# Kernel optimization log

Hardware: AMD Instinct MI355X
Metric: run time of the kernel (lower is better)

The kernel has to match this reference:

```python
import jax, jax.numpy as jnp
import numpy as np

NUM_CLASSES = 4096
FEAT_DIM = 2048
BATCH = 8192


def setup_inputs() -> dict:
    key = jax.random.key(0)
    kx, kl, kc = jax.random.split(key, 3)
    x = jax.random.normal(kx, (BATCH, FEAT_DIM), dtype=jnp.float32)
    labels = jax.random.randint(kl, (BATCH,), 0, NUM_CLASSES, dtype=jnp.int64)
    centers = jax.random.normal(kc, (NUM_CLASSES, FEAT_DIM), dtype=jnp.float32)
    return {"x": x, "labels": labels, "centers": centers}


def reference(x, labels, centers):
    # distmat[b, c] = ||x_b||^2 + ||center_c||^2 - 2 x_b . center_c
    xf = x.astype(jnp.float32)
    cf = centers.astype(jnp.float32)
    x_sq = jnp.sum(xf * xf, axis=1, keepdims=True)          # (B, 1)
    c_sq = jnp.sum(cf * cf, axis=1)[None, :]                 # (1, C)
    distmat = x_sq + c_sq - 2.0 * (xf @ cf.T)                # (B, C)
    # keep only the entry matching each sample's label class
    mask = (labels[:, None] == jnp.arange(NUM_CLASSES)[None, :]).astype(jnp.float32)
    dist = distmat * mask
    # NOTE: torch clamps the masked matrix, so zeroed entries become 1e-12 and
    # still contribute to the sum — replicated faithfully here.
    loss = jnp.clip(dist, 1e-12, 1e12).sum() / x.shape[0]
    return loss
```

## Files before the change

kernel.cpp:

```cpp
#include <hip/hip_runtime.h>


#define BATCH 8192
#define FEAT  2048
#define NCLS  4096
#define BLK   256
#define WAVES_PER_BLK (BLK / 64)
#define NPART (BATCH / WAVES_PER_BLK)

__global__ void __launch_bounds__(BLK)
cl_dist(const float* __restrict__ x,
        const int* __restrict__ labels,
        const float* __restrict__ centers,
        float* __restrict__ part) {
    const int tid  = threadIdx.x;
    const int wid  = tid >> 6;
    const int lane = tid & 63;
    const int b    = blockIdx.x * WAVES_PER_BLK + wid;

    const int lbl = labels[b];

    const float4* __restrict__ xr =
        reinterpret_cast<const float4*>(x + (size_t)b * FEAT);
    const float4* __restrict__ cr =
        reinterpret_cast<const float4*>(centers + (size_t)lbl * FEAT);

    float acc0 = 0.0f, acc1 = 0.0f;
#pragma unroll
    for (int j = 0; j < FEAT / 4 / 64; ++j) {
        const int idx = lane + j * 64;
        const float4 xv = xr[idx];
        const float4 cv = cr[idx];
        const float d0 = xv.x - cv.x;
        const float d1 = xv.y - cv.y;
        const float d2 = xv.z - cv.z;
        const float d3 = xv.w - cv.w;
        acc0 += d0 * d0 + d1 * d1;
        acc1 += d2 * d2 + d3 * d3;
    }
    float acc = acc0 + acc1;

#pragma unroll
    for (int off = 32; off > 0; off >>= 1)
        acc += __shfl_down(acc, off, 64);

    __shared__ float s[WAVES_PER_BLK];
    if (lane == 0) {
        s[wid] = fminf(fmaxf(acc, 1e-12f), 1e12f);
    }
    __syncthreads();

    if (tid == 0)
        part[blockIdx.x] = s[0] + s[1] + s[2] + s[3];
}

__global__ void __launch_bounds__(BLK)
cl_final(const float* __restrict__ part, float* __restrict__ out) {
    const int tid = threadIdx.x;
    float acc = 0.0f;
#pragma unroll
    for (int j = 0; j < NPART / BLK; ++j)
        acc += part[tid + j * BLK];

#pragma unroll
    for (int off = 32; off > 0; off >>= 1)
        acc += __shfl_down(acc, off, 64);

    __shared__ float s[BLK / 64];
    const int wid  = tid >> 6;
    const int lane = tid & 63;
    if (lane == 0) s[wid] = acc;
    __syncthreads();

    if (tid == 0) {
        const float total = s[0] + s[1] + s[2] + s[3];
        out[0] = total / (float)BATCH + (float)(NCLS - 1) * 1e-12f;
    }
}

extern "C" void kernel_launch(void* const* d_in, const int* in_sizes, int n_in,
                              void* d_out, int out_size, void* d_ws, size_t ws_size,
                              hipStream_t stream) {
    const float* x       = (const float*)d_in[0];
    const int*   labels  = (const int*)d_in[1];
    const float* centers = (const float*)d_in[2];
    float* out  = (float*)d_out;
    float* part = (float*)d_ws;

    cl_dist<<<NPART, BLK, 0, stream>>>(x, labels, centers, part);
    cl_final<<<1, BLK, 0, stream>>>(part, out);
}
```

Before: 25.95 us.

## Fuse distance and final reduction into one kernel with spin-wait consumer block

Merges the two kernels into one launch. Block 0 spin-waits with atomic loads and s_sleep on a per-sample partial array, zeroed by a hipMemsetAsync, and sums entries as the producer blocks write their clamped per-sample distances. This removes the second kernel launch and its gap, but adds a memset, polling traffic, and a reliance on nonzero sentinels and forward-progress scheduling of block 0.

```diff
diff --git a/kernel.cpp b/kernel.cpp
--- a/kernel.cpp
+++ b/kernel.cpp
@@ -6,18 +6,48 @@
 #define NCLS  4096
 #define BLK   256
 #define WAVES_PER_BLK (BLK / 64)
-#define NPART (BATCH / WAVES_PER_BLK)
+#define NWBLK (BATCH / WAVES_PER_BLK)
+#define NBLK  (NWBLK + 1)
+#define PER_THREAD (BATCH / BLK)
 
 __global__ void __launch_bounds__(BLK)
-cl_dist(const float* __restrict__ x,
-        const int* __restrict__ labels,
-        const float* __restrict__ centers,
-        float* __restrict__ part) {
+cl_all(const float* __restrict__ x,
+       const int* __restrict__ labels,
+       const float* __restrict__ centers,
+       float* __restrict__ out,
+       float* __restrict__ part) {
     const int tid  = threadIdx.x;
     const int wid  = tid >> 6;
     const int lane = tid & 63;
-    const int b    = blockIdx.x * WAVES_PER_BLK + wid;
+    const int bid  = blockIdx.x;
 
+    __shared__ float s[WAVES_PER_BLK];
+
+    if (bid == 0) {
+        float acc = 0.0f;
+#pragma unroll 1
+        for (int k = 0; k < PER_THREAD; ++k) {
+            const int i = tid + k * BLK;
+            float v;
+            while ((v = __hip_atomic_load(&part[i], __ATOMIC_RELAXED,
+                                          __HIP_MEMORY_SCOPE_AGENT)) == 0.0f) {
+                __builtin_amdgcn_s_sleep(32);
+            }
+            acc += v;
+        }
+#pragma unroll
+        for (int off = 32; off > 0; off >>= 1)
+            acc += __shfl_down(acc, off, 64);
+        if (lane == 0) s[wid] = acc;
+        __syncthreads();
+        if (tid == 0) {
+            const float total = s[0] + s[1] + s[2] + s[3];
+            out[0] = total / (float)BATCH + (float)(NCLS - 1) * 1e-12f;
+        }
+        return;
+    }
+
+    const int b   = (bid - 1) * WAVES_PER_BLK + wid;
     const int lbl = labels[b];
 
     const float4* __restrict__ xr =
@@ -44,37 +74,8 @@
     for (int off = 32; off > 0; off >>= 1)
         acc += __shfl_down(acc, off, 64);
 
-    __shared__ float s[WAVES_PER_BLK];
     if (lane == 0) {
-        s[wid] = fminf(fmaxf(acc, 1e-12f), 1e12f);
-    }
-    __syncthreads();
-
-    if (tid == 0)
-        part[blockIdx.x] = s[0] + s[1] + s[2] + s[3];
-}
-
-__global__ void __launch_bounds__(BLK)
-cl_final(const float* __restrict__ part, float* __restrict__ out) {
-    const int tid = threadIdx.x;
-    float acc = 0.0f;
-#pragma unroll
-    for (int j = 0; j < NPART / BLK; ++j)
-        acc += part[tid + j * BLK];
-
-#pragma unroll
-    for (int off = 32; off > 0; off >>= 1)
-        acc += __shfl_down(acc, off, 64);
-
-    __shared__ float s[BLK / 64];
-    const int wid  = tid >> 6;
-    const int lane = tid & 63;
-    if (lane == 0) s[wid] = acc;
-    __syncthreads();
-
-    if (tid == 0) {
-        const float total = s[0] + s[1] + s[2] + s[3];
-        out[0] = total / (float)BATCH + (float)(NCLS - 1) * 1e-12f;
+        part[b] = fminf(fmaxf(acc, 1e-12f), 1e12f);
     }
 }
 
@@ -87,6 +88,6 @@
     float* out  = (float*)d_out;
     float* part = (float*)d_ws;
 
-    cl_dist<<<NPART, BLK, 0, stream>>>(x, labels, centers, part);
-    cl_final<<<1, BLK, 0, stream>>>(part, out);
+    (void)hipMemsetAsync(d_ws, 0, BATCH * sizeof(float), stream);
+    cl_all<<<NBLK, BLK, 0, stream>>>(x, labels, centers, out, part);
 }
```

Measured after the change: 33.78 us. 30.2% more time.
